# Optimization experiments

Measured on AMD Instinct MI355X. Metric: run time of the kernel, lower is better.

Reference implementation:

```python
import jax, jax.numpy as jnp
import numpy as np

SEQ, D_IN, D_OUT = 8192, 768, 128


def setup_inputs() -> dict:
    key = jax.random.key(0)
    k1, k2, k3, k4 = jax.random.split(key, 4)
    x = jax.random.normal(k1, (SEQ, D_IN), dtype=jnp.float32)
    # torch nn.Linear weights are stored as [d_out, d_in]
    scale = 1.0 / np.sqrt(D_IN)
    w_query = jax.random.normal(k2, (D_OUT, D_IN), dtype=jnp.float32) * scale
    w_key = jax.random.normal(k3, (D_OUT, D_IN), dtype=jnp.float32) * scale
    w_value = jax.random.normal(k4, (D_OUT, D_IN), dtype=jnp.float32) * scale
    return {"x": x, "w_query": w_query, "w_key": w_key, "w_value": w_value}


def reference(x, w_query, w_key, w_value):
    # Linear with bias=False: y = x @ W.T   (W is [d_out, d_in])
    q = x @ w_query.T                      # [N, d_out]
    k = x @ w_key.T                        # [N, d_out]
    v = x @ w_value.T                      # [N, d_out]
    inv_sqrt_d = 1.0 / jnp.sqrt(jnp.float32(k.shape[-1]))
    scores = (q @ k.T) * inv_sqrt_d        # [N, N] -- fully materialized, as in source
    weights = jax.nn.softmax(scores, axis=-1)
    return weights @ v                     # [N, d_out]
```

## Files before the change

kernel.cpp:

```cpp
#include <hip/hip_runtime.h>
#include <stdint.h>

#define SEQ 8192
#define DIN 768
#define DOUT 128

typedef __attribute__((ext_vector_type(8))) short short8;
typedef __attribute__((ext_vector_type(8))) unsigned short ushort8v;
typedef __attribute__((ext_vector_type(4))) float f32x4;

#define CEXPF (1.4426950408889634f * 0.08838834764831845f)

#if __has_builtin(__builtin_amdgcn_exp2f)
#define EXP2(x) __builtin_amdgcn_exp2f(x)
#else
#define EXP2(x) __builtin_exp2f(x)
#endif

__device__ __forceinline__ unsigned short f2bf(float f) {
  return (unsigned short)((__float_as_uint(f) + 0x8000u) >> 16);
}

__device__ __forceinline__ void gload_lds16(const void* g, void* l) {
  __builtin_amdgcn_global_load_lds(
      (const __attribute__((address_space(1))) void*)g,
      (__attribute__((address_space(3))) void*)l, 16, 0, 0);
}

__global__ void conv_kernel(const float* __restrict__ x,
                            const float* __restrict__ wq,
                            const float* __restrict__ wk,
                            const float* __restrict__ wv,
                            unsigned short* __restrict__ xb,
                            unsigned short* __restrict__ Wb) {
  int b = blockIdx.x;
  if (b < 6144) {
    int idx4 = (b * 256 + threadIdx.x) * 4;
    float4 v = *(const float4*)(x + idx4);
    ushort4 o;
    o.x = f2bf(v.x); o.y = f2bf(v.y); o.z = f2bf(v.z); o.w = f2bf(v.w);
    *(ushort4*)(xb + idx4) = o;
  } else {
    int idx4 = ((b - 6144) * 256 + threadIdx.x) * 4;
    int z = idx4 / (DOUT * DIN);
    int rem = idx4 - z * (DOUT * DIN);
    const float* src = (z == 0) ? wq : (z == 1) ? wk : wv;
    float4 v = *(const float4*)(src + rem);
    float sc = (z == 0) ? CEXPF : 1.0f;
    ushort4 o;
    o.x = f2bf(v.x * sc); o.y = f2bf(v.y * sc);
    o.z = f2bf(v.z * sc); o.w = f2bf(v.w * sc);
    *(ushort4*)(Wb + idx4) = o;
  }
}

__launch_bounds__(256, 2)
__global__ void qkv_kernel(const unsigned short* __restrict__ xb,
                           const unsigned short* __restrict__ Wb,
                           unsigned short* __restrict__ Qb,
                           unsigned short* __restrict__ Kb,
                           unsigned short* __restrict__ Vtb) {
  __shared__ unsigned char lds[65536];

  const int t    = threadIdx.x;
  const int wave = t >> 6;
  const int lane = t & 63;
  const int g    = lane >> 4;
  const int r    = lane & 15;
  const int z    = blockIdx.y;
  const int m0   = blockIdx.x * 128;
  const unsigned short* Wz = Wb + (size_t)z * DOUT * DIN;

  auto stage = [&](int buf, int kb) {
    unsigned char* xs = lds + buf * 32768;
    unsigned char* ws = xs + 16384;
#pragma unroll
    for (int c = 0; c < 4; c++) {
      int ci  = (wave * 4 + c) * 64 + lane;
      int row = ci >> 3, ch = ci & 7;
      int sc  = (ch ^ (row & 7)) << 3;
      gload_lds16(xb + (size_t)(m0 + row) * DIN + kb + sc,
                  xs + ((wave * 4 + c) << 10) + (lane << 4));
      gload_lds16(Wz + (size_t)row * DIN + kb + sc,
                  ws + ((wave * 4 + c) << 10) + (lane << 4));
    }
  };

  f32x4 acc[8][2];
#pragma unroll
  for (int mt = 0; mt < 8; mt++)
#pragma unroll
    for (int nt = 0; nt < 2; nt++) acc[mt][nt] = 0.f;

  stage(0, 0);
  asm volatile("s_waitcnt vmcnt(0)" ::: "memory");
  __builtin_amdgcn_s_barrier();
  asm volatile("" ::: "memory");

#pragma unroll 1
  for (int s = 0; s < 12; s++) {
    const int cur = s & 1;
    if (s < 11) stage(cur ^ 1, (s + 1) * 64);
    unsigned char* xs = lds + cur * 32768;
    unsigned char* ws = xs + 16384;
    __builtin_amdgcn_s_setprio(1);
#pragma unroll
    for (int kc = 0; kc < 2; kc++) {
      short8 bfr[2];
#pragma unroll
      for (int nt = 0; nt < 2; nt++) {
        int row = wave * 32 + nt * 16 + r;
        bfr[nt] = *(const short8*)(xs + row * 128 + (((kc * 4 + g) ^ (row & 7)) << 4));
      }
#pragma unroll
      for (int mt = 0; mt < 8; mt++) {
        int oc = mt * 16 + r;
        short8 afr = *(const short8*)(ws + oc * 128 + (((kc * 4 + g) ^ (oc & 7)) << 4));
        acc[mt][0] = __builtin_amdgcn_mfma_f32_16x16x32_bf16(afr, bfr[0], acc[mt][0], 0, 0, 0);
        acc[mt][1] = __builtin_amdgcn_mfma_f32_16x16x32_bf16(afr, bfr[1], acc[mt][1], 0, 0, 0);
      }
    }
    __builtin_amdgcn_s_setprio(0);
    asm volatile("s_waitcnt vmcnt(0)" ::: "memory");
    __builtin_amdgcn_s_barrier();
    asm volatile("" ::: "memory");
  }

  if (z < 2) {
    unsigned short* out = (z == 0) ? Qb : Kb;
#pragma unroll
    for (int mt = 0; mt < 8; mt++)
#pragma unroll
      for (int nt = 0; nt < 2; nt++) {
        ushort4 o;
        o.x = f2bf(acc[mt][nt][0]); o.y = f2bf(acc[mt][nt][1]);
        o.z = f2bf(acc[mt][nt][2]); o.w = f2bf(acc[mt][nt][3]);
        *(ushort4*)(out + (size_t)(m0 + wave * 32 + nt * 16 + r) * DOUT + mt * 16 + g * 4) = o;
      }
  } else {
    unsigned short* ct = (unsigned short*)(lds + wave * 8704);
#pragma unroll
    for (int mt = 0; mt < 8; mt++)
#pragma unroll
      for (int nt = 0; nt < 2; nt++) {
        ushort4 o;
        o.x = f2bf(acc[mt][nt][0]); o.y = f2bf(acc[mt][nt][1]);
        o.z = f2bf(acc[mt][nt][2]); o.w = f2bf(acc[mt][nt][3]);
        *(ushort4*)&ct[(nt * 16 + r) * 136 + mt * 16 + g * 4] = o;
      }
    __syncthreads();
#pragma unroll
    for (int pass = 0; pass < 8; pass++) {
      int col = pass * 16 + (lane >> 2);
      int ch  = lane & 3;
      ushort8v a;
#pragma unroll
      for (int i = 0; i < 8; i++) a[i] = ct[(ch * 8 + i) * 136 + col];
      *(ushort8v*)(Vtb + (size_t)col * SEQ + m0 + wave * 32 + ch * 8) = a;
    }
  }
}

__launch_bounds__(256, 2)
__global__ void attn_kernel(const unsigned short* __restrict__ Qb,
                            const unsigned short* __restrict__ Kb,
                            const unsigned short* __restrict__ Vtb,
                            float* __restrict__ Opart,
                            float* __restrict__ lpart) {
  __shared__ unsigned char lds[74752];

  const int t    = threadIdx.x;
  const int wave = t >> 6;
  const int lane = t & 63;
  const int g    = lane >> 4;
  const int r    = lane & 15;
  unsigned short* Pl = (unsigned short*)(lds + 65536 + wave * 2304);

  const int qb = blockIdx.x;
  const int sp = blockIdx.y;
  const int q0 = qb * 128 + wave * 32;
  const int kvbase = sp * 1024;

  auto stageK = [&](int buf, int kv0) {
    unsigned char* Kl = lds + buf * 16384;
#pragma unroll
    for (int c = 0; c < 4; c++) {
      int idx = (wave * 4 + c) * 64 + lane;
      int krow = idx >> 4, kch = idx & 15;
      gload_lds16(Kb + ((size_t)(kv0 + krow) << 7) + ((kch ^ (krow & 15)) << 3),
                  Kl + ((wave * 4 + c) << 10) + (lane << 4));
    }
  };
  auto stageV = [&](int buf, int kv0) {
    unsigned char* Vl = lds + 32768 + buf * 16384;
#pragma unroll
    for (int c = 0; c < 4; c++) {
      int idx = (wave * 4 + c) * 64 + lane;
      int d = idx >> 3, c2 = idx & 7;
      gload_lds16(Vtb + (size_t)d * SEQ + kv0 + ((c2 ^ (d & 7)) << 3),
                  Vl + ((wave * 4 + c) << 10) + (lane << 4));
    }
  };

  short8 qf[2][4];
#pragma unroll
  for (int nt = 0; nt < 2; nt++)
#pragma unroll
    for (int kc = 0; kc < 4; kc++)
      qf[nt][kc] = *(const short8*)(Qb + (size_t)(q0 + nt * 16 + r) * DOUT + kc * 32 + g * 8);

  short8 onesf;
#pragma unroll
  for (int j = 0; j < 8; j++) onesf[j] = (r == 0) ? (short)0x3F80 : (short)0;

  f32x4 oacc[2][8];
  f32x4 lacc[2];
#pragma unroll
  for (int st = 0; st < 2; st++) {
    lacc[st] = 0.f;
#pragma unroll
    for (int n = 0; n < 8; n++) oacc[st][n] = 0.f;
  }

  stageK(0, kvbase);
  stageV(0, kvbase);
  asm volatile("s_waitcnt vmcnt(0)" ::: "memory");
  __builtin_amdgcn_s_barrier();
  asm volatile("" ::: "memory");

#pragma unroll 1
  for (int it = 0; it < 16; it++) {
    const int cur = it & 1;
    if (it < 15) {
      stageK(cur ^ 1, kvbase + (it + 1) * 64);
      stageV(cur ^ 1, kvbase + (it + 1) * 64);
    }
    unsigned char* Kl = lds + cur * 16384;
    unsigned char* Vl = lds + 32768 + cur * 16384;

    f32x4 sf[4][2];
#pragma unroll
    for (int mt = 0; mt < 4; mt++)
#pragma unroll
      for (int nt = 0; nt < 2; nt++) sf[mt][nt] = 0.f;
    __builtin_amdgcn_s_setprio(1);
#pragma unroll
    for (int mt = 0; mt < 4; mt++) {
      int row = mt * 16 + r;
#pragma unroll
      for (int kc = 0; kc < 4; kc++) {
        short8 kf = *(const short8*)(Kl + row * 256 + (((kc * 4 + g) ^ (row & 15)) << 4));
        sf[mt][0] = __builtin_amdgcn_mfma_f32_16x16x32_bf16(kf, qf[0][kc], sf[mt][0], 0, 0, 0);
        sf[mt][1] = __builtin_amdgcn_mfma_f32_16x16x32_bf16(kf, qf[1][kc], sf[mt][1], 0, 0, 0);
      }
    }
    __builtin_amdgcn_s_setprio(0);

    short8 pf[2][2];
#pragma unroll
    for (int st = 0; st < 2; st++) {
#pragma unroll
      for (int mt = 0; mt < 4; mt++) {
        ushort4 p;
        p.x = f2bf(EXP2(sf[mt][st][0]));
        p.y = f2bf(EXP2(sf[mt][st][1]));
        p.z = f2bf(EXP2(sf[mt][st][2]));
        p.w = f2bf(EXP2(sf[mt][st][3]));
        *(ushort4*)(Pl + r * 72 + mt * 16 + g * 4) = p;
      }
#pragma unroll
      for (int c2 = 0; c2 < 2; c2++)
        pf[st][c2] = *(const short8*)(Pl + r * 72 + c2 * 32 + g * 8);
    }

    __builtin_amdgcn_s_setprio(1);
#pragma unroll
    for (int nt = 0; nt < 8; nt++) {
      int d = nt * 16 + r;
#pragma unroll
      for (int c2 = 0; c2 < 2; c2++) {
        short8 vf = *(const short8*)(Vl + d * 128 + (((c2 * 4 + g) ^ (d & 7)) << 4));
        oacc[0][nt] = __builtin_amdgcn_mfma_f32_16x16x32_bf16(pf[0][c2], vf, oacc[0][nt], 0, 0, 0);
        oacc[1][nt] = __builtin_amdgcn_mfma_f32_16x16x32_bf16(pf[1][c2], vf, oacc[1][nt], 0, 0, 0);
      }
    }
#pragma unroll
    for (int st = 0; st < 2; st++) {
      lacc[st] = __builtin_amdgcn_mfma_f32_16x16x32_bf16(pf[st][0], onesf, lacc[st], 0, 0, 0);
      lacc[st] = __builtin_amdgcn_mfma_f32_16x16x32_bf16(pf[st][1], onesf, lacc[st], 0, 0, 0);
    }
    __builtin_amdgcn_s_setprio(0);

    asm volatile("s_waitcnt vmcnt(0)" ::: "memory");
    __builtin_amdgcn_s_barrier();
    asm volatile("" ::: "memory");
  }

  const size_t pbase = (size_t)sp * SEQ;
#pragma unroll
  for (int st = 0; st < 2; st++)
#pragma unroll
    for (int rr = 0; rr < 4; rr++) {
      int qrow = q0 + st * 16 + g * 4 + rr;
#pragma unroll
      for (int nt = 0; nt < 8; nt++)
        Opart[(pbase + qrow) * DOUT + nt * 16 + r] = oacc[st][nt][rr];
      if (r == 0) lpart[pbase + qrow] = lacc[st][rr];
    }
}

__global__ void combine_kernel(const float* __restrict__ Opart,
                               const float* __restrict__ lpart,
                               float* __restrict__ out) {
  int idx = blockIdx.x * 256 + threadIdx.x;
  int s   = idx >> 5;
  int d4  = (idx & 31) * 4;
  float L = 0.f;
  f32x4 acc = 0.f;
#pragma unroll
  for (int p = 0; p < 8; p++) {
    L += lpart[p * SEQ + s];
    acc += *(const f32x4*)(Opart + ((size_t)p * SEQ + s) * DOUT + d4);
  }
  f32x4 res = acc * (1.0f / L);
  *(f32x4*)(out + (size_t)s * DOUT + d4) = res;
}

extern "C" void kernel_launch(void* const* d_in, const int* in_sizes, int n_in,
                              void* d_out, int out_size, void* d_ws, size_t ws_size,
                              hipStream_t stream) {
  const float* x  = (const float*)d_in[0];
  const float* wq = (const float*)d_in[1];
  const float* wk = (const float*)d_in[2];
  const float* wv = (const float*)d_in[3];
  float* out = (float*)d_out;

  unsigned short* Qb  = (unsigned short*)d_ws;
  unsigned short* Kb  = Qb + (size_t)SEQ * DOUT;
  unsigned short* Vtb = Kb + (size_t)SEQ * DOUT;
  float* Opart = (float*)(Vtb + (size_t)SEQ * DOUT);
  float* lpart = Opart + (size_t)8 * SEQ * DOUT;
  unsigned short* Wb  = (unsigned short*)Opart;
  unsigned short* xb  = Wb + (size_t)3 * DOUT * DIN;
  if (ws_size < (size_t)(6291456 + 33554432 + 262144)) return;

  conv_kernel<<<dim3(6432), 256, 0, stream>>>(x, wq, wk, wv, xb, Wb);
  qkv_kernel<<<dim3(64, 3), 256, 0, stream>>>(xb, Wb, Qb, Kb, Vtb);
  attn_kernel<<<dim3(64, 8), 256, 0, stream>>>(Qb, Kb, Vtb, Opart, lpart);
  combine_kernel<<<dim3(1024), 256, 0, stream>>>(Opart, lpart, out);
}
```

Baseline: 133.2 us.

## Use 8 waves of 16 query rows with 32-key tiles in attention kernel

The attention kernel now runs 512 threads per block. Each wave owns 16 query rows instead of 32, and the KV tile is halved to 32 keys, which shrinks LDS use and per-thread accumulators. Launch bounds rise to 512 threads and 4 blocks so more waves are resident to hide latency. In exchange, each K/V tile is reused by fewer MFMAs per LDS load, and there are twice as many loop iterations and barriers.

```diff
diff --git a/kernel.cpp b/kernel.cpp
--- a/kernel.cpp
+++ b/kernel.cpp
@@ -161,66 +161,57 @@
   }
 }
 
-__launch_bounds__(256, 2)
+__launch_bounds__(512, 4)
 __global__ void attn_kernel(const unsigned short* __restrict__ Qb,
                             const unsigned short* __restrict__ Kb,
                             const unsigned short* __restrict__ Vtb,
                             float* __restrict__ Opart,
                             float* __restrict__ lpart) {
-  __shared__ unsigned char lds[74752];
+  __shared__ unsigned char lds[43008];
 
   const int t    = threadIdx.x;
   const int wave = t >> 6;
   const int lane = t & 63;
   const int g    = lane >> 4;
   const int r    = lane & 15;
-  unsigned short* Pl = (unsigned short*)(lds + 65536 + wave * 2304);
+  unsigned short* Pl = (unsigned short*)(lds + 32768 + wave * 1280);
 
   const int qb = blockIdx.x;
   const int sp = blockIdx.y;
-  const int q0 = qb * 128 + wave * 32;
+  const int q0 = qb * 128 + wave * 16;
   const int kvbase = sp * 1024;
 
   auto stageK = [&](int buf, int kv0) {
-    unsigned char* Kl = lds + buf * 16384;
-#pragma unroll
-    for (int c = 0; c < 4; c++) {
-      int idx = (wave * 4 + c) * 64 + lane;
-      int krow = idx >> 4, kch = idx & 15;
-      gload_lds16(Kb + ((size_t)(kv0 + krow) << 7) + ((kch ^ (krow & 15)) << 3),
-                  Kl + ((wave * 4 + c) << 10) + (lane << 4));
-    }
+    unsigned char* KL = lds + buf * 8192;
+    int idx = (wave << 6) + lane;
+    int krow = idx >> 4, kch = idx & 15;
+    gload_lds16(Kb + ((size_t)(kv0 + krow) << 7) + ((kch ^ (krow & 15)) << 3),
+                KL + (idx << 4));
   };
   auto stageV = [&](int buf, int kv0) {
-    unsigned char* Vl = lds + 32768 + buf * 16384;
-#pragma unroll
-    for (int c = 0; c < 4; c++) {
-      int idx = (wave * 4 + c) * 64 + lane;
-      int d = idx >> 3, c2 = idx & 7;
-      gload_lds16(Vtb + (size_t)d * SEQ + kv0 + ((c2 ^ (d & 7)) << 3),
-                  Vl + ((wave * 4 + c) << 10) + (lane << 4));
-    }
+    unsigned char* VL = lds + 16384 + buf * 8192;
+    int idx = (wave << 6) + lane;
+    int d = idx >> 2, c2 = idx & 3;
+    int sd = (d & 3) ^ ((d >> 2) & 3);
+    gload_lds16(Vtb + (size_t)d * SEQ + kv0 + ((c2 ^ sd) << 3),
+                VL + (idx << 4));
   };
 
-  short8 qf[2][4];
-#pragma unroll
-  for (int nt = 0; nt < 2; nt++)
-#pragma unroll
-    for (int kc = 0; kc < 4; kc++)
-      qf[nt][kc] = *(const short8*)(Qb + (size_t)(q0 + nt * 16 + r) * DOUT + kc * 32 + g * 8);
+  short8 qf[4];
+#pragma unroll
+  for (int kc = 0; kc < 4; kc++)
+    qf[kc] = *(const short8*)(Qb + (size_t)(q0 + r) * DOUT + kc * 32 + g * 8);
 
   short8 onesf;
 #pragma unroll
   for (int j = 0; j < 8; j++) onesf[j] = (r == 0) ? (short)0x3F80 : (short)0;
 
-  f32x4 oacc[2][8];
-  f32x4 lacc[2];
-#pragma unroll
-  for (int st = 0; st < 2; st++) {
-    lacc[st] = 0.f;
-#pragma unroll
-    for (int n = 0; n < 8; n++) oacc[st][n] = 0.f;
-  }
+  f32x4 oacc[8];
+  f32x4 lacc = 0.f;
+#pragma unroll
+  for (int n = 0; n < 8; n++) oacc[n] = 0.f;
+
+  const int sdr = (r & 3) ^ ((r >> 2) & 3);
 
   stageK(0, kvbase);
   stageV(0, kvbase);
@@ -229,66 +220,48 @@
   asm volatile("" ::: "memory");
 
 #pragma unroll 1
-  for (int it = 0; it < 16; it++) {
+  for (int it = 0; it < 32; it++) {
     const int cur = it & 1;
-    if (it < 15) {
-      stageK(cur ^ 1, kvbase + (it + 1) * 64);
-      stageV(cur ^ 1, kvbase + (it + 1) * 64);
-    }
-    unsigned char* Kl = lds + cur * 16384;
-    unsigned char* Vl = lds + 32768 + cur * 16384;
-
-    f32x4 sf[4][2];
-#pragma unroll
-    for (int mt = 0; mt < 4; mt++)
-#pragma unroll
-      for (int nt = 0; nt < 2; nt++) sf[mt][nt] = 0.f;
+    if (it < 31) {
+      stageK(cur ^ 1, kvbase + (it + 1) * 32);
+      stageV(cur ^ 1, kvbase + (it + 1) * 32);
+    }
+    unsigned char* KL = lds + cur * 8192;
+    unsigned char* VL = lds + 16384 + cur * 8192;
+
+    f32x4 sf[2];
+    sf[0] = 0.f; sf[1] = 0.f;
     __builtin_amdgcn_s_setprio(1);
 #pragma unroll
-    for (int mt = 0; mt < 4; mt++) {
+    for (int mt = 0; mt < 2; mt++) {
       int row = mt * 16 + r;
 #pragma unroll
       for (int kc = 0; kc < 4; kc++) {
-        short8 kf = *(const short8*)(Kl + row * 256 + (((kc * 4 + g) ^ (row & 15)) << 4));
-        sf[mt][0] = __builtin_amdgcn_mfma_f32_16x16x32_bf16(kf, qf[0][kc], sf[mt][0], 0, 0, 0);
-        sf[mt][1] = __builtin_amdgcn_mfma_f32_16x16x32_bf16(kf, qf[1][kc], sf[mt][1], 0, 0, 0);
+        short8 kf = *(const short8*)(KL + row * 256 + (((kc * 4 + g) ^ r) << 4));
+        sf[mt] = __builtin_amdgcn_mfma_f32_16x16x32_bf16(kf, qf[kc], sf[mt], 0, 0, 0);
       }
     }
     __builtin_amdgcn_s_setprio(0);
 
-    short8 pf[2][2];
-#pragma unroll
-    for (int st = 0; st < 2; st++) {
-#pragma unroll
-      for (int mt = 0; mt < 4; mt++) {
-        ushort4 p;
-        p.x = f2bf(EXP2(sf[mt][st][0]));
-        p.y = f2bf(EXP2(sf[mt][st][1]));
-        p.z = f2bf(EXP2(sf[mt][st][2]));
-        p.w = f2bf(EXP2(sf[mt][st][3]));
-        *(ushort4*)(Pl + r * 72 + mt * 16 + g * 4) = p;
-      }
-#pragma unroll
-      for (int c2 = 0; c2 < 2; c2++)
-        pf[st][c2] = *(const short8*)(Pl + r * 72 + c2 * 32 + g * 8);
-    }
+#pragma unroll
+    for (int mt = 0; mt < 2; mt++) {
+      ushort4 p;
+      p.x = f2bf(EXP2(sf[mt][0]));
+      p.y = f2bf(EXP2(sf[mt][1]));
+      p.z = f2bf(EXP2(sf[mt][2]));
+      p.w = f2bf(EXP2(sf[mt][3]));
+      *(ushort4*)(Pl + r * 40 + mt * 16 + g * 4) = p;
+    }
+    short8 pf = *(const short8*)(Pl + r * 40 + g * 8);
 
     __builtin_amdgcn_s_setprio(1);
 #pragma unroll
     for (int nt = 0; nt < 8; nt++) {
       int d = nt * 16 + r;
-#pragma unroll
-      for (int c2 = 0; c2 < 2; c2++) {
-        short8 vf = *(const short8*)(Vl + d * 128 + (((c2 * 4 + g) ^ (d & 7)) << 4));
-        oacc[0][nt] = __builtin_amdgcn_mfma_f32_16x16x32_bf16(pf[0][c2], vf, oacc[0][nt], 0, 0, 0);
-        oacc[1][nt] = __builtin_amdgcn_mfma_f32_16x16x32_bf16(pf[1][c2], vf, oacc[1][nt], 0, 0, 0);
-      }
-    }
-#pragma unroll
-    for (int st = 0; st < 2; st++) {
-      lacc[st] = __builtin_amdgcn_mfma_f32_16x16x32_bf16(pf[st][0], onesf, lacc[st], 0, 0, 0);
-      lacc[st] = __builtin_amdgcn_mfma_f32_16x16x32_bf16(pf[st][1], onesf, lacc[st], 0, 0, 0);
-    }
+      short8 vf = *(const short8*)(VL + d * 64 + ((g ^ sdr) << 4));
+      oacc[nt] = __builtin_amdgcn_mfma_f32_16x16x32_bf16(pf, vf, oacc[nt], 0, 0, 0);
+    }
+    lacc = __builtin_amdgcn_mfma_f32_16x16x32_bf16(pf, onesf, lacc, 0, 0, 0);
     __builtin_amdgcn_s_setprio(0);
 
     asm volatile("s_waitcnt vmcnt(0)" ::: "memory");
@@ -298,15 +271,13 @@
 
   const size_t pbase = (size_t)sp * SEQ;
 #pragma unroll
-  for (int st = 0; st < 2; st++)
-#pragma unroll
-    for (int rr = 0; rr < 4; rr++) {
-      int qrow = q0 + st * 16 + g * 4 + rr;
-#pragma unroll
-      for (int nt = 0; nt < 8; nt++)
-        Opart[(pbase + qrow) * DOUT + nt * 16 + r] = oacc[st][nt][rr];
-      if (r == 0) lpart[pbase + qrow] = lacc[st][rr];
-    }
+  for (int rr = 0; rr < 4; rr++) {
+    int qrow = q0 + g * 4 + rr;
+#pragma unroll
+    for (int nt = 0; nt < 8; nt++)
+      Opart[(pbase + qrow) * DOUT + nt * 16 + r] = oacc[nt][rr];
+    if (r == 0) lpart[pbase + qrow] = lacc[rr];
+  }
 }
 
 __global__ void combine_kernel(const float* __restrict__ Opart,
@@ -346,6 +317,6 @@
 
   conv_kernel<<<dim3(6432), 256, 0, stream>>>(x, wq, wk, wv, xb, Wb);
   qkv_kernel<<<dim3(64, 3), 256, 0, stream>>>(xb, Wb, Qb, Kb, Vtb);
-  attn_kernel<<<dim3(64, 8), 256, 0, stream>>>(Qb, Kb, Vtb, Opart, lpart);
+  attn_kernel<<<dim3(64, 8), 512, 0, stream>>>(Qb, Kb, Vtb, Opart, lpart);
   combine_kernel<<<dim3(1024), 256, 0, stream>>>(Opart, lpart, out);
 }
```

Measured after the change: 138.7 us. 4.2% more time.

## Fuse split-KV combine into attention kernel via last-block atomic counter

Applied to the files above, without the earlier changes.

Removes the separate combine kernel launch. Each attention block now bumps a per-query-block counter after writing its partial output, and the last of the 8 split blocks reduces the partials and normalises them into the output. The counters are zeroed in the conversion kernel. This saves a launch and its tail, but the reduction work is concentrated on 64 blocks and adds fences plus coherent atomic loads.

```diff
diff --git a/kernel.cpp b/kernel.cpp
--- a/kernel.cpp
+++ b/kernel.cpp
@@ -27,13 +27,20 @@
       (__attribute__((address_space(3))) void*)l, 16, 0, 0);
 }
 
+__device__ __forceinline__ float cohload(const float* p) {
+  return __hip_atomic_load(p, __ATOMIC_RELAXED, __HIP_MEMORY_SCOPE_AGENT);
+}
+
 __global__ void conv_kernel(const float* __restrict__ x,
                             const float* __restrict__ wq,
                             const float* __restrict__ wk,
                             const float* __restrict__ wv,
                             unsigned short* __restrict__ xb,
-                            unsigned short* __restrict__ Wb) {
+                            unsigned short* __restrict__ Wb,
+                            int* __restrict__ cnt) {
   int b = blockIdx.x;
+  if (b == 6431 && threadIdx.x < 64)
+    __hip_atomic_store(&cnt[threadIdx.x], 0, __ATOMIC_RELAXED, __HIP_MEMORY_SCOPE_AGENT);
   if (b < 6144) {
     int idx4 = (b * 256 + threadIdx.x) * 4;
     float4 v = *(const float4*)(x + idx4);
@@ -166,8 +173,11 @@
                             const unsigned short* __restrict__ Kb,
                             const unsigned short* __restrict__ Vtb,
                             float* __restrict__ Opart,
-                            float* __restrict__ lpart) {
+                            float* __restrict__ lpart,
+                            int* __restrict__ cnt,
+                            float* __restrict__ out) {
   __shared__ unsigned char lds[74752];
+  __shared__ int is_last;
 
   const int t    = threadIdx.x;
   const int wave = t >> 6;
@@ -307,23 +317,42 @@
         Opart[(pbase + qrow) * DOUT + nt * 16 + r] = oacc[st][nt][rr];
       if (r == 0) lpart[pbase + qrow] = lacc[st][rr];
     }
-}
-
-__global__ void combine_kernel(const float* __restrict__ Opart,
-                               const float* __restrict__ lpart,
-                               float* __restrict__ out) {
-  int idx = blockIdx.x * 256 + threadIdx.x;
-  int s   = idx >> 5;
-  int d4  = (idx & 31) * 4;
-  float L = 0.f;
-  f32x4 acc = 0.f;
-#pragma unroll
-  for (int p = 0; p < 8; p++) {
-    L += lpart[p * SEQ + s];
-    acc += *(const f32x4*)(Opart + ((size_t)p * SEQ + s) * DOUT + d4);
-  }
-  f32x4 res = acc * (1.0f / L);
-  *(f32x4*)(out + (size_t)s * DOUT + d4) = res;
+
+  __threadfence();
+  __syncthreads();
+  if (t == 0)
+    is_last = (__hip_atomic_fetch_add(&cnt[qb], 1, __ATOMIC_ACQ_REL,
+                                      __HIP_MEMORY_SCOPE_AGENT) == 7);
+  __syncthreads();
+  if (!is_last) return;
+  __threadfence();
+  float* Linv = (float*)lds;
+  if (t < 128) {
+    float L = 0.f;
+#pragma unroll
+    for (int p = 0; p < 8; p++) L += cohload(&lpart[(size_t)p * SEQ + qb * 128 + t]);
+    Linv[t] = 1.0f / L;
+  }
+  __syncthreads();
+#pragma unroll 1
+  for (int k2 = 0; k2 < 16; k2++) {
+    int linear = k2 * 256 + t;
+    int srow = linear >> 5;
+    int d4 = (linear & 31) * 4;
+    const float* base = Opart + ((size_t)qb * 128 + srow) * DOUT + d4;
+    float a0 = 0.f, a1 = 0.f, a2 = 0.f, a3 = 0.f;
+#pragma unroll
+    for (int p = 0; p < 8; p++) {
+      const float* bp = base + (size_t)p * SEQ * DOUT;
+      a0 += cohload(bp + 0);
+      a1 += cohload(bp + 1);
+      a2 += cohload(bp + 2);
+      a3 += cohload(bp + 3);
+    }
+    float linv = Linv[srow];
+    f32x4 res; res[0] = a0 * linv; res[1] = a1 * linv; res[2] = a2 * linv; res[3] = a3 * linv;
+    *(f32x4*)(out + ((size_t)(qb * 128 + srow)) * DOUT + d4) = res;
+  }
 }
 
 extern "C" void kernel_launch(void* const* d_in, const int* in_sizes, int n_in,
@@ -340,12 +369,12 @@
   unsigned short* Vtb = Kb + (size_t)SEQ * DOUT;
   float* Opart = (float*)(Vtb + (size_t)SEQ * DOUT);
   float* lpart = Opart + (size_t)8 * SEQ * DOUT;
+  int*   cnt   = (int*)(lpart + (size_t)8 * SEQ);
   unsigned short* Wb  = (unsigned short*)Opart;
   unsigned short* xb  = Wb + (size_t)3 * DOUT * DIN;
-  if (ws_size < (size_t)(6291456 + 33554432 + 262144)) return;
-
-  conv_kernel<<<dim3(6432), 256, 0, stream>>>(x, wq, wk, wv, xb, Wb);
+  if (ws_size < (size_t)(6291456 + 33554432 + 262144 + 4096)) return;
+
+  conv_kernel<<<dim3(6432), 256, 0, stream>>>(x, wq, wk, wv, xb, Wb, cnt);
   qkv_kernel<<<dim3(64, 3), 256, 0, stream>>>(xb, Wb, Qb, Kb, Vtb);
-  attn_kernel<<<dim3(64, 8), 256, 0, stream>>>(Qb, Kb, Vtb, Opart, lpart);
-  combine_kernel<<<dim3(1024), 256, 0, stream>>>(Opart, lpart, out);
-}
+  attn_kernel<<<dim3(64, 8), 256, 0, stream>>>(Qb, Kb, Vtb, Opart, lpart, cnt, out);
+}
```

Measured after the change: 232.8 us. +74.9%, slower.

## Fuse conv, QKV and attention into one cooperative persistent kernel

Applied to the files above, without the earlier changes.

Merges the bf16 conversion, QKV projection and attention kernels into a single cooperative kernel of 512 blocks, separated by grid-wide syncs, so three kernel launches and their inter-kernel gaps become one. The conversion loop becomes grid-strided, and only 192 blocks do QKV work while the rest wait at the barrier. It falls back to the separate launches if the cooperative launch fails. In exchange it adds grid-sync cost, lets 320 blocks sit idle during the projection, and raises the projection kernel's LDS allocation to the attention size.

```diff
diff --git a/kernel.cpp b/kernel.cpp
--- a/kernel.cpp
+++ b/kernel.cpp
@@ -1,5 +1,8 @@
 #include <hip/hip_runtime.h>
+#include <hip/hip_cooperative_groups.h>
 #include <stdint.h>
+
+namespace cg = cooperative_groups;
 
 #define SEQ 8192
 #define DIN 768
@@ -27,13 +30,14 @@
       (__attribute__((address_space(3))) void*)l, 16, 0, 0);
 }
 
-__global__ void conv_kernel(const float* __restrict__ x,
-                            const float* __restrict__ wq,
-                            const float* __restrict__ wk,
-                            const float* __restrict__ wv,
-                            unsigned short* __restrict__ xb,
-                            unsigned short* __restrict__ Wb) {
-  int b = blockIdx.x;
+
+__device__ __forceinline__ void conv_body(int b,
+                                          const float* __restrict__ x,
+                                          const float* __restrict__ wq,
+                                          const float* __restrict__ wk,
+                                          const float* __restrict__ wv,
+                                          unsigned short* __restrict__ xb,
+                                          unsigned short* __restrict__ Wb) {
   if (b < 6144) {
     int idx4 = (b * 256 + threadIdx.x) * 4;
     float4 v = *(const float4*)(x + idx4);
@@ -54,21 +58,18 @@
   }
 }
 
-__launch_bounds__(256, 2)
-__global__ void qkv_kernel(const unsigned short* __restrict__ xb,
-                           const unsigned short* __restrict__ Wb,
-                           unsigned short* __restrict__ Qb,
-                           unsigned short* __restrict__ Kb,
-                           unsigned short* __restrict__ Vtb) {
-  __shared__ unsigned char lds[65536];
-
+__device__ __forceinline__ void qkv_body(int bx, int z, unsigned char* lds,
+                                         const unsigned short* __restrict__ xb,
+                                         const unsigned short* __restrict__ Wb,
+                                         unsigned short* __restrict__ Qb,
+                                         unsigned short* __restrict__ Kb,
+                                         unsigned short* __restrict__ Vtb) {
   const int t    = threadIdx.x;
   const int wave = t >> 6;
   const int lane = t & 63;
   const int g    = lane >> 4;
   const int r    = lane & 15;
-  const int z    = blockIdx.y;
-  const int m0   = blockIdx.x * 128;
+  const int m0   = bx * 128;
   const unsigned short* Wz = Wb + (size_t)z * DOUT * DIN;
 
   auto stage = [&](int buf, int kb) {
@@ -161,6 +162,191 @@
   }
 }
 
+__device__ __forceinline__ void attn_body(int qb, int sp, unsigned char* lds,
+                                          const unsigned short* __restrict__ Qb,
+                                          const unsigned short* __restrict__ Kb,
+                                          const unsigned short* __restrict__ Vtb,
+                                          float* __restrict__ Opart,
+                                          float* __restrict__ lpart) {
+  const int t    = threadIdx.x;
+  const int wave = t >> 6;
+  const int lane = t & 63;
+  const int g    = lane >> 4;
+  const int r    = lane & 15;
+  unsigned short* Pl = (unsigned short*)(lds + 65536 + wave * 2304);
+
+  const int q0 = qb * 128 + wave * 32;
+  const int kvbase = sp * 1024;
+
+  auto stageK = [&](int buf, int kv0) {
+    unsigned char* Kl = lds + buf * 16384;
+#pragma unroll
+    for (int c = 0; c < 4; c++) {
+      int idx = (wave * 4 + c) * 64 + lane;
+      int krow = idx >> 4, kch = idx & 15;
+      gload_lds16(Kb + ((size_t)(kv0 + krow) << 7) + ((kch ^ (krow & 15)) << 3),
+                  Kl + ((wave * 4 + c) << 10) + (lane << 4));
+    }
+  };
+  auto stageV = [&](int buf, int kv0) {
+    unsigned char* Vl = lds + 32768 + buf * 16384;
+#pragma unroll
+    for (int c = 0; c < 4; c++) {
+      int idx = (wave * 4 + c) * 64 + lane;
+      int d = idx >> 3, c2 = idx & 7;
+      gload_lds16(Vtb + (size_t)d * SEQ + kv0 + ((c2 ^ (d & 7)) << 3),
+                  Vl + ((wave * 4 + c) << 10) + (lane << 4));
+    }
+  };
+
+  short8 qf[2][4];
+#pragma unroll
+  for (int nt = 0; nt < 2; nt++)
+#pragma unroll
+    for (int kc = 0; kc < 4; kc++)
+      qf[nt][kc] = *(const short8*)(Qb + (size_t)(q0 + nt * 16 + r) * DOUT + kc * 32 + g * 8);
+
+  short8 onesf;
+#pragma unroll
+  for (int j = 0; j < 8; j++) onesf[j] = (r == 0) ? (short)0x3F80 : (short)0;
+
+  f32x4 oacc[2][8];
+  f32x4 lacc[2];
+#pragma unroll
+  for (int st = 0; st < 2; st++) {
+    lacc[st] = 0.f;
+#pragma unroll
+    for (int n = 0; n < 8; n++) oacc[st][n] = 0.f;
+  }
+
+  stageK(0, kvbase);
+  stageV(0, kvbase);
+  asm volatile("s_waitcnt vmcnt(0)" ::: "memory");
+  __builtin_amdgcn_s_barrier();
+  asm volatile("" ::: "memory");
+
+#pragma unroll 1
+  for (int it = 0; it < 16; it++) {
+    const int cur = it & 1;
+    if (it < 15) {
+      stageK(cur ^ 1, kvbase + (it + 1) * 64);
+      stageV(cur ^ 1, kvbase + (it + 1) * 64);
+    }
+    unsigned char* Kl = lds + cur * 16384;
+    unsigned char* Vl = lds + 32768 + cur * 16384;
+
+    f32x4 sf[4][2];
+#pragma unroll
+    for (int mt = 0; mt < 4; mt++)
+#pragma unroll
+      for (int nt = 0; nt < 2; nt++) sf[mt][nt] = 0.f;
+    __builtin_amdgcn_s_setprio(1);
+#pragma unroll
+    for (int mt = 0; mt < 4; mt++) {
+      int row = mt * 16 + r;
+#pragma unroll
+      for (int kc = 0; kc < 4; kc++) {
+        short8 kf = *(const short8*)(Kl + row * 256 + (((kc * 4 + g) ^ (row & 15)) << 4));
+        sf[mt][0] = __builtin_amdgcn_mfma_f32_16x16x32_bf16(kf, qf[0][kc], sf[mt][0], 0, 0, 0);
+        sf[mt][1] = __builtin_amdgcn_mfma_f32_16x16x32_bf16(kf, qf[1][kc], sf[mt][1], 0, 0, 0);
+      }
+    }
+    __builtin_amdgcn_s_setprio(0);
+
+    short8 pf[2][2];
+#pragma unroll
+    for (int st = 0; st < 2; st++) {
+#pragma unroll
+      for (int mt = 0; mt < 4; mt++) {
+        ushort4 p;
+        p.x = f2bf(EXP2(sf[mt][st][0]));
+        p.y = f2bf(EXP2(sf[mt][st][1]));
+        p.z = f2bf(EXP2(sf[mt][st][2]));
+        p.w = f2bf(EXP2(sf[mt][st][3]));
+        *(ushort4*)(Pl + r * 72 + mt * 16 + g * 4) = p;
+      }
+#pragma unroll
+      for (int c2 = 0; c2 < 2; c2++)
+        pf[st][c2] = *(const short8*)(Pl + r * 72 + c2 * 32 + g * 8);
+    }
+
+    __builtin_amdgcn_s_setprio(1);
+#pragma unroll
+    for (int nt = 0; nt < 8; nt++) {
+      int d = nt * 16 + r;
+#pragma unroll
+      for (int c2 = 0; c2 < 2; c2++) {
+        short8 vf = *(const short8*)(Vl + d * 128 + (((c2 * 4 + g) ^ (d & 7)) << 4));
+        oacc[0][nt] = __builtin_amdgcn_mfma_f32_16x16x32_bf16(pf[0][c2], vf, oacc[0][nt], 0, 0, 0);
+        oacc[1][nt] = __builtin_amdgcn_mfma_f32_16x16x32_bf16(pf[1][c2], vf, oacc[1][nt], 0, 0, 0);
+      }
+    }
+#pragma unroll
+    for (int st = 0; st < 2; st++) {
+      lacc[st] = __builtin_amdgcn_mfma_f32_16x16x32_bf16(pf[st][0], onesf, lacc[st], 0, 0, 0);
+      lacc[st] = __builtin_amdgcn_mfma_f32_16x16x32_bf16(pf[st][1], onesf, lacc[st], 0, 0, 0);
+    }
+    __builtin_amdgcn_s_setprio(0);
+
+    asm volatile("s_waitcnt vmcnt(0)" ::: "memory");
+    __builtin_amdgcn_s_barrier();
+    asm volatile("" ::: "memory");
+  }
+
+  const size_t pbase = (size_t)sp * SEQ;
+#pragma unroll
+  for (int st = 0; st < 2; st++)
+#pragma unroll
+    for (int rr = 0; rr < 4; rr++) {
+      int qrow = q0 + st * 16 + g * 4 + rr;
+#pragma unroll
+      for (int nt = 0; nt < 8; nt++)
+        Opart[(pbase + qrow) * DOUT + nt * 16 + r] = oacc[st][nt][rr];
+      if (r == 0) lpart[pbase + qrow] = lacc[st][rr];
+    }
+}
+
+__launch_bounds__(256, 2)
+__global__ void mega_kernel(const float* __restrict__ x,
+                            const float* __restrict__ wq,
+                            const float* __restrict__ wk,
+                            const float* __restrict__ wv,
+                            unsigned short* __restrict__ xb,
+                            unsigned short* __restrict__ Wb,
+                            unsigned short* __restrict__ Qb,
+                            unsigned short* __restrict__ Kb,
+                            unsigned short* __restrict__ Vtb,
+                            float* __restrict__ Opart,
+                            float* __restrict__ lpart) {
+  __shared__ unsigned char lds[74752];
+  for (int b = blockIdx.x; b < 6432; b += 512)
+    conv_body(b, x, wq, wk, wv, xb, Wb);
+  cg::this_grid().sync();
+  if (blockIdx.x < 192)
+    qkv_body(blockIdx.x & 63, blockIdx.x >> 6, lds, xb, Wb, Qb, Kb, Vtb);
+  cg::this_grid().sync();
+  attn_body(blockIdx.x & 63, blockIdx.x >> 6, lds, Qb, Kb, Vtb, Opart, lpart);
+}
+
+__global__ void conv_kernel(const float* __restrict__ x,
+                            const float* __restrict__ wq,
+                            const float* __restrict__ wk,
+                            const float* __restrict__ wv,
+                            unsigned short* __restrict__ xb,
+                            unsigned short* __restrict__ Wb) {
+  conv_body(blockIdx.x, x, wq, wk, wv, xb, Wb);
+}
+
+__launch_bounds__(256, 2)
+__global__ void qkv_kernel(const unsigned short* __restrict__ xb,
+                           const unsigned short* __restrict__ Wb,
+                           unsigned short* __restrict__ Qb,
+                           unsigned short* __restrict__ Kb,
+                           unsigned short* __restrict__ Vtb) {
+  __shared__ unsigned char lds[65536];
+  qkv_body(blockIdx.x, blockIdx.y, lds, xb, Wb, Qb, Kb, Vtb);
+}
+
 __launch_bounds__(256, 2)
 __global__ void attn_kernel(const unsigned short* __restrict__ Qb,
                             const unsigned short* __restrict__ Kb,
@@ -168,145 +354,7 @@
                             float* __restrict__ Opart,
                             float* __restrict__ lpart) {
   __shared__ unsigned char lds[74752];
-
-  const int t    = threadIdx.x;
-  const int wave = t >> 6;
-  const int lane = t & 63;
-  const int g    = lane >> 4;
-  const int r    = lane & 15;
-  unsigned short* Pl = (unsigned short*)(lds + 65536 + wave * 2304);
-
-  const int qb = blockIdx.x;
-  const int sp = blockIdx.y;
-  const int q0 = qb * 128 + wave * 32;
-  const int kvbase = sp * 1024;
-
-  auto stageK = [&](int buf, int kv0) {
-    unsigned char* Kl = lds + buf * 16384;
-#pragma unroll
-    for (int c = 0; c < 4; c++) {
-      int idx = (wave * 4 + c) * 64 + lane;
-      int krow = idx >> 4, kch = idx & 15;
-      gload_lds16(Kb + ((size_t)(kv0 + krow) << 7) + ((kch ^ (krow & 15)) << 3),
-                  Kl + ((wave * 4 + c) << 10) + (lane << 4));
-    }
-  };
-  auto stageV = [&](int buf, int kv0) {
-    unsigned char* Vl = lds + 32768 + buf * 16384;
-#pragma unroll
-    for (int c = 0; c < 4; c++) {
-      int idx = (wave * 4 + c) * 64 + lane;
-      int d = idx >> 3, c2 = idx & 7;
-      gload_lds16(Vtb + (size_t)d * SEQ + kv0 + ((c2 ^ (d & 7)) << 3),
-                  Vl + ((wave * 4 + c) << 10) + (lane << 4));
-    }
-  };
-
-  short8 qf[2][4];
-#pragma unroll
-  for (int nt = 0; nt < 2; nt++)
-#pragma unroll
-    for (int kc = 0; kc < 4; kc++)
-      qf[nt][kc] = *(const short8*)(Qb + (size_t)(q0 + nt * 16 + r) * DOUT + kc * 32 + g * 8);
-
-  short8 onesf;
-#pragma unroll
-  for (int j = 0; j < 8; j++) onesf[j] = (r == 0) ? (short)0x3F80 : (short)0;
-
-  f32x4 oacc[2][8];
-  f32x4 lacc[2];
-#pragma unroll
-  for (int st = 0; st < 2; st++) {
-    lacc[st] = 0.f;
-#pragma unroll
-    for (int n = 0; n < 8; n++) oacc[st][n] = 0.f;
-  }
-
-  stageK(0, kvbase);
-  stageV(0, kvbase);
-  asm volatile("s_waitcnt vmcnt(0)" ::: "memory");
-  __builtin_amdgcn_s_barrier();
-  asm volatile("" ::: "memory");
-
-#pragma unroll 1
-  for (int it = 0; it < 16; it++) {
-    const int cur = it & 1;
-    if (it < 15) {
-      stageK(cur ^ 1, kvbase + (it + 1) * 64);
-      stageV(cur ^ 1, kvbase + (it + 1) * 64);
-    }
-    unsigned char* Kl = lds + cur * 16384;
-    unsigned char* Vl = lds + 32768 + cur * 16384;
-
-    f32x4 sf[4][2];
-#pragma unroll
-    for (int mt = 0; mt < 4; mt++)
-#pragma unroll
-      for (int nt = 0; nt < 2; nt++) sf[mt][nt] = 0.f;
-    __builtin_amdgcn_s_setprio(1);
-#pragma unroll
-    for (int mt = 0; mt < 4; mt++) {
-      int row = mt * 16 + r;
-#pragma unroll
-      for (int kc = 0; kc < 4; kc++) {
-        short8 kf = *(const short8*)(Kl + row * 256 + (((kc * 4 + g) ^ (row & 15)) << 4));
-        sf[mt][0] = __builtin_amdgcn_mfma_f32_16x16x32_bf16(kf, qf[0][kc], sf[mt][0], 0, 0, 0);
-        sf[mt][1] = __builtin_amdgcn_mfma_f32_16x16x32_bf16(kf, qf[1][kc], sf[mt][1], 0, 0, 0);
-      }
-    }
-    __builtin_amdgcn_s_setprio(0);
-
-    short8 pf[2][2];
-#pragma unroll
-    for (int st = 0; st < 2; st++) {
-#pragma unroll
-      for (int mt = 0; mt < 4; mt++) {
-        ushort4 p;
-        p.x = f2bf(EXP2(sf[mt][st][0]));
-        p.y = f2bf(EXP2(sf[mt][st][1]));
-        p.z = f2bf(EXP2(sf[mt][st][2]));
-        p.w = f2bf(EXP2(sf[mt][st][3]));
-        *(ushort4*)(Pl + r * 72 + mt * 16 + g * 4) = p;
-      }
-#pragma unroll
-      for (int c2 = 0; c2 < 2; c2++)
-        pf[st][c2] = *(const short8*)(Pl + r * 72 + c2 * 32 + g * 8);
-    }
-
-    __builtin_amdgcn_s_setprio(1);
-#pragma unroll
-    for (int nt = 0; nt < 8; nt++) {
-      int d = nt * 16 + r;
-#pragma unroll
-      for (int c2 = 0; c2 < 2; c2++) {
-        short8 vf = *(const short8*)(Vl + d * 128 + (((c2 * 4 + g) ^ (d & 7)) << 4));
-        oacc[0][nt] = __builtin_amdgcn_mfma_f32_16x16x32_bf16(pf[0][c2], vf, oacc[0][nt], 0, 0, 0);
-        oacc[1][nt] = __builtin_amdgcn_mfma_f32_16x16x32_bf16(pf[1][c2], vf, oacc[1][nt], 0, 0, 0);
-      }
-    }
-#pragma unroll
-    for (int st = 0; st < 2; st++) {
-      lacc[st] = __builtin_amdgcn_mfma_f32_16x16x32_bf16(pf[st][0], onesf, lacc[st], 0, 0, 0);
-      lacc[st] = __builtin_amdgcn_mfma_f32_16x16x32_bf16(pf[st][1], onesf, lacc[st], 0, 0, 0);
-    }
-    __builtin_amdgcn_s_setprio(0);
-
-    asm volatile("s_waitcnt vmcnt(0)" ::: "memory");
-    __builtin_amdgcn_s_barrier();
-    asm volatile("" ::: "memory");
-  }
-
-  const size_t pbase = (size_t)sp * SEQ;
-#pragma unroll
-  for (int st = 0; st < 2; st++)
-#pragma unroll
-    for (int rr = 0; rr < 4; rr++) {
-      int qrow = q0 + st * 16 + g * 4 + rr;
-#pragma unroll
-      for (int nt = 0; nt < 8; nt++)
-        Opart[(pbase + qrow) * DOUT + nt * 16 + r] = oacc[st][nt][rr];
-      if (r == 0) lpart[pbase + qrow] = lacc[st][rr];
-    }
+  attn_body(blockIdx.x, blockIdx.y, lds, Qb, Kb, Vtb, Opart, lpart);
 }
 
 __global__ void combine_kernel(const float* __restrict__ Opart,
@@ -344,8 +392,16 @@
   unsigned short* xb  = Wb + (size_t)3 * DOUT * DIN;
   if (ws_size < (size_t)(6291456 + 33554432 + 262144)) return;
 
-  conv_kernel<<<dim3(6432), 256, 0, stream>>>(x, wq, wk, wv, xb, Wb);
-  qkv_kernel<<<dim3(64, 3), 256, 0, stream>>>(xb, Wb, Qb, Kb, Vtb);
-  attn_kernel<<<dim3(64, 8), 256, 0, stream>>>(Qb, Kb, Vtb, Opart, lpart);
+  void* margs[] = {(void*)&x, (void*)&wq, (void*)&wk, (void*)&wv,
+                   (void*)&xb, (void*)&Wb, (void*)&Qb, (void*)&Kb, (void*)&Vtb,
+                   (void*)&Opart, (void*)&lpart};
+  hipError_t err = hipLaunchCooperativeKernel((const void*)mega_kernel,
+                                              dim3(512), dim3(256),
+                                              margs, 0, stream);
+  if (err != hipSuccess) {
+    conv_kernel<<<dim3(6432), 256, 0, stream>>>(x, wq, wk, wv, xb, Wb);
+    qkv_kernel<<<dim3(64, 3), 256, 0, stream>>>(xb, Wb, Qb, Kb, Vtb);
+    attn_kernel<<<dim3(64, 8), 256, 0, stream>>>(Qb, Kb, Vtb, Opart, lpart);
+  }
   combine_kernel<<<dim3(1024), 256, 0, stream>>>(Opart, lpart, out);
 }
```

Result: slower. 273.0 us (+105.1%).
